# Kernel optimization log

Hardware: AMD Instinct MI355X
Metric: run time of the kernel (lower is better)

## Reference

```python
import jax, jax.numpy as jnp
import numpy as np

B, N, DIN, DOUT, H, DH, DC, NL, L = 8, 256, 64, 64, 8, 8, 64, 32, 2
SCALE = DH ** -0.5  # out_dim-per-head scaling used by both attention variants


def _ln(x, g, b):
    m = jnp.mean(x, -1, keepdims=True)
    v = jnp.mean((x - m) ** 2, -1, keepdims=True)
    return (x - m) * jax.lax.rsqrt(v + 1e-5) * g + b


def _cross_attn(x, ctx, mask_b, wq, wkv, wo, bo):
    # CrossAttentionLayer: standard softmax attention with clamp(-5,5)
    b, n, _ = x.shape
    m = ctx.shape[1]
    q = (x @ wq).reshape(b, n, H, DH).transpose(0, 2, 1, 3)
    k, v = jnp.split(ctx @ wkv, 2, axis=-1)
    k = k.reshape(b, m, H, DH).transpose(0, 2, 1, 3)
    v = v.reshape(b, m, H, DH).transpose(0, 2, 1, 3)
    sim = jnp.einsum('bhid,bhjd->bhij', q, k) * SCALE
    if mask_b is not None:
        sim = jnp.where(mask_b[:, None, None, :], sim, -jnp.finfo(sim.dtype).max)
    sim = jnp.clip(sim, -5.0, 5.0)
    attn = jax.nn.softmax(sim, axis=-1)
    out = jnp.einsum('bhij,bhjd->bhid', attn, v)
    out = out.transpose(0, 2, 1, 3).reshape(b, n, H * DH)
    return out @ wo + bo


def _mha_edge(p, e, k_RW, mask, wq, wk, we, wv):
    # GraphiT MultiHeadAttentionLayer with edge features + k_RW attention PE
    Q = (p @ wq).reshape(B, N, H, DH)
    K = (p @ wk).reshape(B, N, H, DH) * SCALE
    V = (p @ wv).reshape(B, N, H, DH).transpose(0, 2, 1, 3)  # [B,H,N,d]
    E = (e @ we).reshape(B, N, N, H, DH)
    scores = jnp.einsum('bihk,bjhk,bijhk->bhij', Q, K, E)
    scores = jnp.exp(scores - jnp.max(scores, axis=(-2, -1), keepdims=True))
    scores = scores * mask[:, None, :, None] * mask[:, None, None, :]
    scores = scores * k_RW
    denom = jnp.clip(jnp.sum(scores, -1, keepdims=True), 1e-6, None)
    out = jnp.einsum('bhij,bhjd->bhid', scores, V) / denom
    return out.transpose(0, 2, 1, 3).reshape(B, N, H * DH)


def setup_inputs() -> dict:
    key = jax.random.key(0)
    ks = jax.random.split(key, 32)
    rn = lambda k, s: jax.random.normal(k, s, dtype=jnp.float32)
    inp = {
        'h': rn(ks[0], (B, N, DIN)),
        'p': rn(ks[1], (B, N, DIN)),
        'e': rn(ks[2], (B, N, N, DIN)),
        'k_RW': jax.random.uniform(ks[3], (B, 1, N, N), dtype=jnp.float32),
        'queries': rn(ks[4], (B, NL, DC)),
        'mask': jnp.ones((B, N), dtype=jnp.float32),
        # attention_p (MultiHeadAttentionLayer) weights
        'wq_p': rn(ks[5], (DIN, H * DH)) * 0.05,
        'wk_p': rn(ks[6], (DIN, H * DH)) * 0.05,
        'we_p': rn(ks[7], (DIN, H * DH)) * 0.05,
        'wv_p': rn(ks[8], (DIN, H * DH)) * 0.05,
        'wo_p': rn(ks[9], (DOUT, DOUT)) * 0.05,
        # cross_attention_h (queries attend to nodes)
        'cq_wq': rn(ks[10], (DC, H * DH)) * 0.05,
        'cq_wkv': rn(ks[11], (DIN, 2 * H * DH)) * 0.05,
        'cq_wo': rn(ks[12], (H * DH, DC)) * 0.05,
        'cq_bo': jnp.zeros((DC,), dtype=jnp.float32),
        # L_cross latent self-attention layers (stacked)
        'sa_wq': rn(ks[13], (L, DC, H * DH)) * 0.05,
        'sa_wkv': rn(ks[14], (L, DC, 2 * H * DH)) * 0.05,
        'sa_wo': rn(ks[15], (L, H * DH, DC)) * 0.05,
        'sa_bo': jnp.zeros((L, DC), dtype=jnp.float32),
        # O_queries, norms, FFN
        'oq_w': rn(ks[16], (DC, DC)) * 0.05,
        'ln1_g': jnp.ones((DC,), dtype=jnp.float32),
        'ln1_b': jnp.zeros((DC,), dtype=jnp.float32),
        'ffn_w1': rn(ks[17], (DC, 2 * DC)) * 0.05,
        'ffn_w2': rn(ks[18], (2 * DC, DC)) * 0.05,
        'ln2_g': jnp.ones((DC,), dtype=jnp.float32),
        'ln2_b': jnp.zeros((DC,), dtype=jnp.float32),
    }
    return inp


def reference(h, p, e, k_RW, queries, mask,
              wq_p, wk_p, we_p, wv_p, wo_p,
              cq_wq, cq_wkv, cq_wo, cq_bo,
              sa_wq, sa_wkv, sa_wo, sa_bo,
              oq_w, ln1_g, ln1_b, ffn_w1, ffn_w2, ln2_g, ln2_b):
    # forward_p: update positional encoding via edge-modulated attention
    p_attn = _mha_edge(p, e, k_RW, mask, wq_p, wk_p, we_p, wv_p)
    p_new = p + jnp.tanh(p_attn @ wo_p)  # residual, no dropout (eval)
    # combine node features with updated PE (use_node_pe='sum')
    h_c = h + p_new
    mask_b = mask > 0.5
    # perceiver cross-attention: latents attend to nodes
    q = queries + _cross_attn(queries, h_c, mask_b, cq_wq, cq_wkv, cq_wo, cq_bo)
    # L_cross latent self-attention blocks with residual
    for i in range(L):
        q = q + _cross_attn(q, q, None, sa_wq[i], sa_wkv[i], sa_wo[i], sa_bo[i])
    # O_queries projection + layer norm
    q = _ln(q @ oq_w, ln1_g, ln1_b)
    # feed-forward block on queries
    ff = jax.nn.relu(q @ ffn_w1) @ ffn_w2
    q = _ln(q + ff, ln2_g, ln2_b)
    return q
```

## Files before the change

### kernel.cpp

```cpp
#include <hip/hip_runtime.h>
#include <hip/hip_bf16.h>
#include <math.h>

typedef __bf16 bf16x8 __attribute__((ext_vector_type(8)));
typedef float floatx4 __attribute__((ext_vector_type(4)));

#define ATT_SCALE 0.35355339059327373f

__device__ __forceinline__ __bf16 f2b(float x) { return (__bf16)x; }

__global__ void k_proj(const float* __restrict__ p,
                       const float* __restrict__ wq, const float* __restrict__ wk,
                       const float* __restrict__ wv,
                       float* __restrict__ Q, float* __restrict__ Ks,
                       float* __restrict__ V) {
  int blk = blockIdx.x, t = threadIdx.x;
  __shared__ float xr[64];
  xr[t] = p[blk * 64 + t];
  __syncthreads();
  float aq = 0.f, ak = 0.f, av = 0.f;
#pragma unroll 8
  for (int c = 0; c < 64; c++) {
    float x = xr[c];
    aq += x * wq[c * 64 + t];
    ak += x * wk[c * 64 + t];
    av += x * wv[c * 64 + t];
  }
  Q[blk * 64 + t] = aq;
  Ks[blk * 64 + t] = ak * ATT_SCALE;
  V[blk * 64 + t] = av;
}

__global__ __launch_bounds__(256) void k_edge(
    const float* __restrict__ e, const float* __restrict__ we,
    const float* __restrict__ krw, const float* __restrict__ mask,
    const float* __restrict__ hin, const float* __restrict__ pin,
    const float* __restrict__ wo, const float* __restrict__ cq_wkv,
    const float* __restrict__ Q, const float* __restrict__ Ks,
    const float* __restrict__ V, float* __restrict__ Kc, float* __restrict__ Vc) {
  int bi = blockIdx.x;
  int b = bi >> 8;
  int t = threadIdx.x;
  int w = t >> 6, l = t & 63;
  int l15 = l & 15, quad = l >> 4, half8 = (l >> 3) & 1, d = l & 7;

  bf16x8 wfrag[4][2];
#pragma unroll
  for (int nt = 0; nt < 4; nt++)
#pragma unroll
    for (int kc = 0; kc < 2; kc++)
#pragma unroll
      for (int jj = 0; jj < 8; jj++)
        wfrag[nt][kc][jj] = f2b(we[(kc * 32 + quad * 8 + jj) * 64 + nt * 16 + l15]);

  float qv[4];
#pragma unroll
  for (int nt = 0; nt < 4; nt++) qv[nt] = Q[bi * 64 + nt * 16 + l15];
  float mi = mask[bi];

  float aout[4] = {0.f, 0.f, 0.f, 0.f};
  float aden[4] = {0.f, 0.f, 0.f, 0.f};

  for (int mt = 0; mt < 4; mt++) {
    int j0 = w * 64 + mt * 16;
    const float* ep = e + ((long)bi * 256 + j0 + l15) * 64 + quad * 8;
    float4 ea = *reinterpret_cast<const float4*>(ep);
    float4 eb4 = *reinterpret_cast<const float4*>(ep + 4);
    float4 ec = *reinterpret_cast<const float4*>(ep + 32);
    float4 ed4 = *reinterpret_cast<const float4*>(ep + 36);
    bf16x8 a0, a1;
    a0[0] = f2b(ea.x); a0[1] = f2b(ea.y); a0[2] = f2b(ea.z); a0[3] = f2b(ea.w);
    a0[4] = f2b(eb4.x); a0[5] = f2b(eb4.y); a0[6] = f2b(eb4.z); a0[7] = f2b(eb4.w);
    a1[0] = f2b(ec.x); a1[1] = f2b(ec.y); a1[2] = f2b(ec.z); a1[3] = f2b(ec.w);
    a1[4] = f2b(ed4.x); a1[5] = f2b(ed4.y); a1[6] = f2b(ed4.z); a1[7] = f2b(ed4.w);

    int jr0 = j0 + quad * 4;
    float krw_r[4], mj_r[4];
#pragma unroll
    for (int r = 0; r < 4; r++) {
      krw_r[r] = krw[(long)bi * 256 + jr0 + r];
      mj_r[r] = mask[b * 256 + jr0 + r];
    }
#pragma unroll
    for (int nt = 0; nt < 4; nt++) {
      floatx4 acc = {0.f, 0.f, 0.f, 0.f};
      acc = __builtin_amdgcn_mfma_f32_16x16x32_bf16(a0, wfrag[nt][0], acc, 0, 0, 0);
      acc = __builtin_amdgcn_mfma_f32_16x16x32_bf16(a1, wfrag[nt][1], acc, 0, 0, 0);
      int hk = nt * 16 + l15;
      int hbase = hk & 56;
#pragma unroll
      for (int r = 0; r < 4; r++) {
        int jr = jr0 + r;
        float s = acc[r] * qv[nt] * Ks[(b * 256 + jr) * 64 + hk];
        s += __shfl_xor(s, 1);
        s += __shfl_xor(s, 2);
        s += __shfl_xor(s, 4);
        float wg = __expf(s) * krw_r[r] * mj_r[r];
        aden[nt] += wg;
        aout[nt] += wg * V[(b * 256 + jr) * 64 + hbase + d];
      }
    }
  }
#pragma unroll
  for (int nt = 0; nt < 4; nt++) {
    float o = aout[nt], dn = aden[nt];
    o += __shfl_xor(o, 16); o += __shfl_xor(o, 32);
    dn += __shfl_xor(dn, 16); dn += __shfl_xor(dn, 32);
    aout[nt] = o; aden[nt] = dn;
  }

  __shared__ float red[4][64];
  __shared__ float redden[4][8];
  __shared__ float pav[64];
  __shared__ float hcl[64];
  if (l < 16) {
#pragma unroll
    for (int nt = 0; nt < 4; nt++) {
      int head = nt * 2 + half8;
      red[w][head * 8 + d] = aout[nt];
      if (d == 0) redden[w][head] = aden[nt];
    }
  }
  __syncthreads();
  if (t < 64) {
    int head = t >> 3;
    float num = red[0][t] + red[1][t] + red[2][t] + red[3][t];
    float den = redden[0][head] + redden[1][head] + redden[2][head] + redden[3][head];
    num *= mi;
    den = fmaxf(den * mi, 1e-6f);
    pav[t] = num / den;
  }
  __syncthreads();
  if (t < 64) {
    float a = 0.f;
#pragma unroll 8
    for (int c = 0; c < 64; c++) a += pav[c] * wo[c * 64 + t];
    hcl[t] = hin[bi * 64 + t] + pin[bi * 64 + t] + tanhf(a);
  }
  __syncthreads();
  if (t < 128) {
    float a = 0.f;
#pragma unroll 8
    for (int c = 0; c < 64; c++) a += hcl[c] * cq_wkv[c * 128 + t];
    if (t < 64) Kc[bi * 64 + t] = a;
    else        Vc[bi * 64 + t - 64] = a;
  }
}

__global__ __launch_bounds__(1024) void k_tail(
    const float* __restrict__ quer, const float* __restrict__ Kc,
    const float* __restrict__ Vc, const float* __restrict__ mask,
    const float* __restrict__ cq_wq, const float* __restrict__ cq_wo,
    const float* __restrict__ cq_bo,
    const float* __restrict__ sa_wq, const float* __restrict__ sa_wkv,
    const float* __restrict__ sa_wo, const float* __restrict__ sa_bo,
    const float* __restrict__ oq_w, const float* __restrict__ g1,
    const float* __restrict__ b1, const float* __restrict__ w1,
    const float* __restrict__ w2, const float* __restrict__ g2,
    const float* __restrict__ b2v, float* __restrict__ out) {
  int b = blockIdx.x;
  int t = threadIdx.x;

  __shared__ float pool[8704];
  __shared__ float sq[32 * 68];
  __shared__ float sx[32 * 68];
  __shared__ float soc[32 * 68];
  __shared__ float smask[256];

  {
    int r0 = t >> 5, c2 = (t & 31) * 2;
    sq[r0 * 68 + c2]     = quer[b * 2048 + r0 * 64 + c2];
    sq[r0 * 68 + c2 + 1] = quer[b * 2048 + r0 * 64 + c2 + 1];
    if (t < 256) smask[t] = mask[b * 256 + t];
  }
  __syncthreads();

#pragma unroll
  for (int half = 0; half < 2; half++) {
    int o = t + half * 1024, rr = o >> 6, c = o & 63;
    float a = 0.f;
#pragma unroll 8
    for (int k = 0; k < 64; k++) a += sq[rr * 68 + k] * cq_wq[k * 64 + c];
    sx[rr * 68 + c] = a;
  }
  __syncthreads();

  int r = t >> 5, h = (t >> 2) & 7, s = t & 3;
  {
    float qv8[8];
#pragma unroll
    for (int dd = 0; dd < 8; dd++) qv8[dd] = sx[r * 68 + h * 8 + dd];
    float num[8] = {0.f, 0.f, 0.f, 0.f, 0.f, 0.f, 0.f, 0.f};
    float den = 0.f;
    for (int qtr = 0; qtr < 4; qtr++) {
      {
        int jl = t >> 4, c4 = (t & 15) * 4;
        long row = (long)(b * 256 + qtr * 64 + jl) * 64 + c4;
        float4 kk = *reinterpret_cast<const float4*>(Kc + row);
        float4 vv = *reinterpret_cast<const float4*>(Vc + row);
        *reinterpret_cast<float4*>(&pool[jl * 68 + c4]) = kk;
        *reinterpret_cast<float4*>(&pool[64 * 68 + jl * 68 + c4]) = vv;
      }
      __syncthreads();
#pragma unroll
      for (int jj = 0; jj < 16; jj++) {
        int jl = jj * 4 + s;
        const float* kp = &pool[jl * 68 + h * 8];
        float4 k0 = *reinterpret_cast<const float4*>(kp);
        float4 k1 = *reinterpret_cast<const float4*>(kp + 4);
        float sc = qv8[0] * k0.x + qv8[1] * k0.y + qv8[2] * k0.z + qv8[3] * k0.w
                 + qv8[4] * k1.x + qv8[5] * k1.y + qv8[6] * k1.z + qv8[7] * k1.w;
        sc *= ATT_SCALE;
        sc = (smask[qtr * 64 + jl] > 0.5f) ? sc : -1e30f;
        sc = fminf(fmaxf(sc, -5.f), 5.f);
        float ex = __expf(sc);
        den += ex;
        const float* vp = &pool[64 * 68 + jl * 68 + h * 8];
        float4 v0 = *reinterpret_cast<const float4*>(vp);
        float4 v1 = *reinterpret_cast<const float4*>(vp + 4);
        num[0] += ex * v0.x; num[1] += ex * v0.y; num[2] += ex * v0.z; num[3] += ex * v0.w;
        num[4] += ex * v1.x; num[5] += ex * v1.y; num[6] += ex * v1.z; num[7] += ex * v1.w;
      }
      __syncthreads();
    }
    den += __shfl_xor(den, 1); den += __shfl_xor(den, 2);
#pragma unroll
    for (int dd = 0; dd < 8; dd++) {
      float v = num[dd];
      v += __shfl_xor(v, 1); v += __shfl_xor(v, 2);
      num[dd] = v;
    }
    if (s == 0) {
      float inv = 1.f / den;
#pragma unroll
      for (int dd = 0; dd < 8; dd++) soc[r * 68 + h * 8 + dd] = num[dd] * inv;
    }
  }
  __syncthreads();

#pragma unroll
  for (int half = 0; half < 2; half++) {
    int o = t + half * 1024, rr = o >> 6, c = o & 63;
    float a = 0.f;
#pragma unroll 8
    for (int k = 0; k < 64; k++) a += soc[rr * 68 + k] * cq_wo[k * 64 + c];
    sq[rr * 68 + c] += a + cq_bo[c];
  }
  __syncthreads();

  for (int layer = 0; layer < 2; layer++) {
    const float* wql = sa_wq + layer * 4096;
    const float* wkvl = sa_wkv + layer * 8192;
    const float* wol = sa_wo + layer * 4096;
    const float* bol = sa_bo + layer * 64;

#pragma unroll
    for (int half = 0; half < 2; half++) {
      int o = t + half * 1024, rr = o >> 6, c = o & 63;
      float a = 0.f;
#pragma unroll 8
      for (int k = 0; k < 64; k++) a += sq[rr * 68 + k] * wql[k * 64 + c];
      sx[rr * 68 + c] = a;
    }
#pragma unroll
    for (int qu = 0; qu < 4; qu++) {
      int o = t + qu * 1024, rr = o >> 7, c = o & 127;
      float a = 0.f;
#pragma unroll 8
      for (int k = 0; k < 64; k++) a += sq[rr * 68 + k] * wkvl[k * 128 + c];
      if (c < 64) pool[rr * 65 + c] = a;
      else        pool[2080 + rr * 65 + (c - 64)] = a;
    }
    __syncthreads();

    {
      float qv[8];
#pragma unroll
      for (int dd = 0; dd < 8; dd++) qv[dd] = sx[r * 68 + h * 8 + dd];
      float nm[8] = {0.f, 0.f, 0.f, 0.f, 0.f, 0.f, 0.f, 0.f};
      float dn = 0.f;
#pragma unroll
      for (int jj = 0; jj < 8; jj++) {
        int j = jj * 4 + s;
        const float* kp = &pool[j * 65 + h * 8];
        float sc = 0.f;
#pragma unroll
        for (int dd = 0; dd < 8; dd++) sc += qv[dd] * kp[dd];
        sc *= ATT_SCALE;
        sc = fminf(fmaxf(sc, -5.f), 5.f);
        float ex = __expf(sc);
        dn += ex;
        const float* vp = &pool[2080 + j * 65 + h * 8];
#pragma unroll
        for (int dd = 0; dd < 8; dd++) nm[dd] += ex * vp[dd];
      }
      dn += __shfl_xor(dn, 1); dn += __shfl_xor(dn, 2);
#pragma unroll
      for (int dd = 0; dd < 8; dd++) {
        float v = nm[dd];
        v += __shfl_xor(v, 1); v += __shfl_xor(v, 2);
        nm[dd] = v;
      }
      if (s == 0) {
        float inv = 1.f / dn;
#pragma unroll
        for (int dd = 0; dd < 8; dd++) soc[r * 68 + h * 8 + dd] = nm[dd] * inv;
      }
    }
    __syncthreads();

#pragma unroll
    for (int half = 0; half < 2; half++) {
      int o = t + half * 1024, rr = o >> 6, c = o & 63;
      float a = 0.f;
#pragma unroll 8
      for (int k = 0; k < 64; k++) a += soc[rr * 68 + k] * wol[k * 64 + c];
      sq[rr * 68 + c] += a + bol[c];
    }
    __syncthreads();
  }

#pragma unroll
  for (int half = 0; half < 2; half++) {
    int o = t + half * 1024, rr = o >> 6, c = o & 63;
    float a = 0.f;
#pragma unroll 8
    for (int k = 0; k < 64; k++) a += sq[rr * 68 + k] * oq_w[k * 64 + c];
    sx[rr * 68 + c] = a;
  }
  __syncthreads();
  {
    int wv = t >> 6, lc = t & 63;
#pragma unroll
    for (int pass = 0; pass < 2; pass++) {
      int rr = wv + pass * 16;
      float x = sx[rr * 68 + lc];
      float m = x;
      for (int off = 1; off < 64; off <<= 1) m += __shfl_xor(m, off);
      m *= (1.f / 64.f);
      float dv = x - m, vv = dv * dv;
      for (int off = 1; off < 64; off <<= 1) vv += __shfl_xor(vv, off);
      vv *= (1.f / 64.f);
      sx[rr * 68 + lc] = dv * rsqrtf(vv + 1e-5f) * g1[lc] + b1[lc];
    }
  }
  __syncthreads();

#pragma unroll
  for (int qu = 0; qu < 4; qu++) {
    int o = t + qu * 1024, rr = o >> 7, c = o & 127;
    float a = 0.f;
#pragma unroll 8
    for (int k = 0; k < 64; k++) a += sx[rr * 68 + k] * w1[k * 128 + c];
    pool[rr * 128 + c] = fmaxf(a, 0.f);
  }
  __syncthreads();

  {
    int wv = t >> 6, lc = t & 63;
#pragma unroll
    for (int pass = 0; pass < 2; pass++) {
      int rr = wv + pass * 16;
      float ff = 0.f;
#pragma unroll 8
      for (int k = 0; k < 128; k++) ff += pool[rr * 128 + k] * w2[k * 64 + lc];
      float z = sx[rr * 68 + lc] + ff;
      float m2 = z;
      for (int off = 1; off < 64; off <<= 1) m2 += __shfl_xor(m2, off);
      m2 *= (1.f / 64.f);
      float dz = z - m2, v2 = dz * dz;
      for (int off = 1; off < 64; off <<= 1) v2 += __shfl_xor(v2, off);
      v2 *= (1.f / 64.f);
      out[b * 2048 + rr * 64 + lc] = dz * rsqrtf(v2 + 1e-5f) * g2[lc] + b2v[lc];
    }
  }
}

extern "C" void kernel_launch(void* const* d_in, const int* in_sizes, int n_in,
                              void* d_out, int out_size, void* d_ws, size_t ws_size,
                              hipStream_t stream) {
  const float* h_in   = (const float*)d_in[0];
  const float* p_in   = (const float*)d_in[1];
  const float* e_in   = (const float*)d_in[2];
  const float* krw    = (const float*)d_in[3];
  const float* quer   = (const float*)d_in[4];
  const float* mask   = (const float*)d_in[5];
  const float* wq_p   = (const float*)d_in[6];
  const float* wk_p   = (const float*)d_in[7];
  const float* we_p   = (const float*)d_in[8];
  const float* wv_p   = (const float*)d_in[9];
  const float* wo_p   = (const float*)d_in[10];
  const float* cq_wq  = (const float*)d_in[11];
  const float* cq_wkv = (const float*)d_in[12];
  const float* cq_wo  = (const float*)d_in[13];
  const float* cq_bo  = (const float*)d_in[14];
  const float* sa_wq  = (const float*)d_in[15];
  const float* sa_wkv = (const float*)d_in[16];
  const float* sa_wo  = (const float*)d_in[17];
  const float* sa_bo  = (const float*)d_in[18];
  const float* oq_w   = (const float*)d_in[19];
  const float* ln1_g  = (const float*)d_in[20];
  const float* ln1_b  = (const float*)d_in[21];
  const float* ffn_w1 = (const float*)d_in[22];
  const float* ffn_w2 = (const float*)d_in[23];
  const float* ln2_g  = (const float*)d_in[24];
  const float* ln2_b  = (const float*)d_in[25];

  float* ws = (float*)d_ws;
  float* Q  = ws;
  float* Ks = Q + 131072;
  float* V  = Ks + 131072;
  float* Kc = V + 131072;
  float* Vc = Kc + 131072;

  k_proj<<<2048, 64, 0, stream>>>(p_in, wq_p, wk_p, wv_p, Q, Ks, V);
  k_edge<<<2048, 256, 0, stream>>>(e_in, we_p, krw, mask, h_in, p_in, wo_p, cq_wkv,
                                   Q, Ks, V, Kc, Vc);
  k_tail<<<8, 1024, 0, stream>>>(quer, Kc, Vc, mask, cq_wq, cq_wo, cq_bo,
                                 sa_wq, sa_wkv, sa_wo, sa_bo, oq_w,
                                 ln1_g, ln1_b, ffn_w1, ffn_w2, ln2_g, ln2_b,
                                 (float*)d_out);
}
```

Before: 373.9 us.

## Stage tail weights in LDS as bf16 and batch rows per thread in projections

k_proj now computes 8 rows per 256-thread block, so each weight load is reused across 8 rows instead of one. k_tail stages every weight matrix into shared memory as bf16 and has each thread compute 2–4 output rows. Cross-attention K/V tiles are kept in LDS as bf16, and the cq_wo weights are staged while the first K/V tile loads. Unroll pragmas are also removed throughout k_edge. This trades precision in the tail for fewer global weight reads and less LDS traffic, and dropping the unroll pragmas in k_edge may change its code generation.

```diff
diff --git a/kernel.cpp b/kernel.cpp
--- a/kernel.cpp
+++ b/kernel.cpp
@@ -9,26 +9,34 @@
 
 __device__ __forceinline__ __bf16 f2b(float x) { return (__bf16)x; }
 
-__global__ void k_proj(const float* __restrict__ p,
+__global__ __launch_bounds__(256) void k_proj(const float* __restrict__ p,
                        const float* __restrict__ wq, const float* __restrict__ wk,
                        const float* __restrict__ wv,
                        float* __restrict__ Q, float* __restrict__ Ks,
                        float* __restrict__ V) {
   int blk = blockIdx.x, t = threadIdx.x;
-  __shared__ float xr[64];
-  xr[t] = p[blk * 64 + t];
-  __syncthreads();
-  float aq = 0.f, ak = 0.f, av = 0.f;
-#pragma unroll 8
-  for (int c = 0; c < 64; c++) {
-    float x = xr[c];
-    aq += x * wq[c * 64 + t];
-    ak += x * wk[c * 64 + t];
-    av += x * wv[c * 64 + t];
-  }
-  Q[blk * 64 + t] = aq;
-  Ks[blk * 64 + t] = ak * ATT_SCALE;
-  V[blk * 64 + t] = av;
+  __shared__ float xr[8][64];
+  {
+    int rr = t >> 5, cc = (t & 31) * 2;
+    float2 pz = *reinterpret_cast<const float2*>(p + blk * 512 + rr * 64 + cc);
+    xr[rr][cc] = pz.x; xr[rr][cc + 1] = pz.y;
+  }
+  __syncthreads();
+  if (t < 192) {
+    int mat = t >> 6, c = t & 63;
+    const float* w = (mat == 0) ? wq : ((mat == 1) ? wk : wv);
+    float acc[8] = {0.f, 0.f, 0.f, 0.f, 0.f, 0.f, 0.f, 0.f};
+#pragma unroll 8
+    for (int k = 0; k < 64; k++) {
+      float wv_ = w[k * 64 + c];
+#pragma unroll
+      for (int r = 0; r < 8; r++) acc[r] += xr[r][k] * wv_;
+    }
+    float* dst = (mat == 0) ? Q : ((mat == 1) ? Ks : V);
+    float sc = (mat == 1) ? ATT_SCALE : 1.f;
+#pragma unroll
+    for (int r = 0; r < 8; r++) dst[(blk * 8 + r) * 64 + c] = acc[r] * sc;
+  }
 }
 
 __global__ __launch_bounds__(256) void k_edge(
@@ -45,16 +53,12 @@
   int l15 = l & 15, quad = l >> 4, half8 = (l >> 3) & 1, d = l & 7;
 
   bf16x8 wfrag[4][2];
-#pragma unroll
   for (int nt = 0; nt < 4; nt++)
-#pragma unroll
     for (int kc = 0; kc < 2; kc++)
-#pragma unroll
       for (int jj = 0; jj < 8; jj++)
         wfrag[nt][kc][jj] = f2b(we[(kc * 32 + quad * 8 + jj) * 64 + nt * 16 + l15]);
 
   float qv[4];
-#pragma unroll
   for (int nt = 0; nt < 4; nt++) qv[nt] = Q[bi * 64 + nt * 16 + l15];
   float mi = mask[bi];
 
@@ -76,19 +80,16 @@
 
     int jr0 = j0 + quad * 4;
     float krw_r[4], mj_r[4];
-#pragma unroll
     for (int r = 0; r < 4; r++) {
       krw_r[r] = krw[(long)bi * 256 + jr0 + r];
       mj_r[r] = mask[b * 256 + jr0 + r];
     }
-#pragma unroll
     for (int nt = 0; nt < 4; nt++) {
       floatx4 acc = {0.f, 0.f, 0.f, 0.f};
       acc = __builtin_amdgcn_mfma_f32_16x16x32_bf16(a0, wfrag[nt][0], acc, 0, 0, 0);
       acc = __builtin_amdgcn_mfma_f32_16x16x32_bf16(a1, wfrag[nt][1], acc, 0, 0, 0);
       int hk = nt * 16 + l15;
       int hbase = hk & 56;
-#pragma unroll
       for (int r = 0; r < 4; r++) {
         int jr = jr0 + r;
         float s = acc[r] * qv[nt] * Ks[(b * 256 + jr) * 64 + hk];
@@ -101,7 +102,6 @@
       }
     }
   }
-#pragma unroll
   for (int nt = 0; nt < 4; nt++) {
     float o = aout[nt], dn = aden[nt];
     o += __shfl_xor(o, 16); o += __shfl_xor(o, 32);
@@ -114,7 +114,6 @@
   __shared__ float pav[64];
   __shared__ float hcl[64];
   if (l < 16) {
-#pragma unroll
     for (int nt = 0; nt < 4; nt++) {
       int head = nt * 2 + half8;
       red[w][head * 8 + d] = aout[nt];
@@ -133,17 +132,31 @@
   __syncthreads();
   if (t < 64) {
     float a = 0.f;
-#pragma unroll 8
     for (int c = 0; c < 64; c++) a += pav[c] * wo[c * 64 + t];
     hcl[t] = hin[bi * 64 + t] + pin[bi * 64 + t] + tanhf(a);
   }
   __syncthreads();
   if (t < 128) {
     float a = 0.f;
-#pragma unroll 8
     for (int c = 0; c < 64; c++) a += hcl[c] * cq_wkv[c * 128 + t];
     if (t < 64) Kc[bi * 64 + t] = a;
     else        Vc[bi * 64 + t - 64] = a;
+  }
+}
+
+template <int NR, int NC, int ST>
+__device__ __forceinline__ void stage_w(const float* __restrict__ g,
+                                        __bf16* wls, int t) {
+  constexpr int PER = (NR * NC) >> 10;
+  int i0 = t * PER;
+  int k = i0 / NC, c0 = i0 % NC;
+  const float* src = g + k * NC + c0;
+  __bf16* dst = wls + k * ST + c0;
+#pragma unroll
+  for (int m = 0; m < PER; m += 4) {
+    float4 v = *reinterpret_cast<const float4*>(src + m);
+    dst[m] = f2b(v.x); dst[m + 1] = f2b(v.y);
+    dst[m + 2] = f2b(v.z); dst[m + 3] = f2b(v.w);
   }
 }
 
@@ -161,65 +174,76 @@
   int b = blockIdx.x;
   int t = threadIdx.x;
 
-  __shared__ float pool[8704];
   __shared__ float sq[32 * 68];
   __shared__ float sx[32 * 68];
-  __shared__ float soc[32 * 68];
+  __shared__ float pool[6400];
   __shared__ float smask[256];
-
-  {
-    int r0 = t >> 5, c2 = (t & 31) * 2;
-    sq[r0 * 68 + c2]     = quer[b * 2048 + r0 * 64 + c2];
-    sq[r0 * 68 + c2 + 1] = quer[b * 2048 + r0 * 64 + c2 + 1];
+  __shared__ __bf16 wls[8448];
+
+  float* soc = pool + 4160;
+  __bf16* kq = reinterpret_cast<__bf16*>(pool);
+  __bf16* vq = kq + 4096;
+
+  const int rr6 = t >> 6, c6 = t & 63;
+  const int r2 = t >> 5, h = (t >> 2) & 7, s = t & 3;
+
+  {
+    float2 qz = *reinterpret_cast<const float2*>(quer + b * 2048 + (t >> 5) * 64 + (t & 31) * 2);
+    sq[(t >> 5) * 68 + (t & 31) * 2] = qz.x;
+    sq[(t >> 5) * 68 + (t & 31) * 2 + 1] = qz.y;
     if (t < 256) smask[t] = mask[b * 256 + t];
-  }
-  __syncthreads();
-
-#pragma unroll
-  for (int half = 0; half < 2; half++) {
-    int o = t + half * 1024, rr = o >> 6, c = o & 63;
-    float a = 0.f;
-#pragma unroll 8
-    for (int k = 0; k < 64; k++) a += sq[rr * 68 + k] * cq_wq[k * 64 + c];
-    sx[rr * 68 + c] = a;
-  }
-  __syncthreads();
-
-  int r = t >> 5, h = (t >> 2) & 7, s = t & 3;
+    stage_w<64, 64, 66>(cq_wq, wls, t);
+  }
+  __syncthreads();
+
+  {
+    float a0 = 0.f, a1 = 0.f;
+#pragma unroll 8
+    for (int k = 0; k < 64; k++) {
+      float wv = (float)wls[k * 66 + c6];
+      a0 += sq[rr6 * 68 + k] * wv;
+      a1 += sq[(rr6 + 16) * 68 + k] * wv;
+    }
+    sx[rr6 * 68 + c6] = a0;
+    sx[(rr6 + 16) * 68 + c6] = a1;
+  }
+  __syncthreads();
+
+  float num[8] = {0.f, 0.f, 0.f, 0.f, 0.f, 0.f, 0.f, 0.f};
+  float den = 0.f;
   {
     float qv8[8];
 #pragma unroll
-    for (int dd = 0; dd < 8; dd++) qv8[dd] = sx[r * 68 + h * 8 + dd];
-    float num[8] = {0.f, 0.f, 0.f, 0.f, 0.f, 0.f, 0.f, 0.f};
-    float den = 0.f;
+    for (int dd = 0; dd < 8; dd++) qv8[dd] = sx[r2 * 68 + h * 8 + dd];
     for (int qtr = 0; qtr < 4; qtr++) {
       {
-        int jl = t >> 4, c4 = (t & 15) * 4;
-        long row = (long)(b * 256 + qtr * 64 + jl) * 64 + c4;
-        float4 kk = *reinterpret_cast<const float4*>(Kc + row);
-        float4 vv = *reinterpret_cast<const float4*>(Vc + row);
-        *reinterpret_cast<float4*>(&pool[jl * 68 + c4]) = kk;
-        *reinterpret_cast<float4*>(&pool[64 * 68 + jl * 68 + c4]) = vv;
-      }
+        int half = t >> 9, idx = t & 511;
+        int jl = idx >> 3, c0 = (idx & 7) * 8;
+        const float* src = (half ? Vc : Kc) + ((long)(b * 256 + qtr * 64 + jl)) * 64 + c0;
+        __bf16* dst = (half ? vq : kq) + jl * 64 + c0;
+        float4 u = *reinterpret_cast<const float4*>(src);
+        float4 v = *reinterpret_cast<const float4*>(src + 4);
+        dst[0] = f2b(u.x); dst[1] = f2b(u.y); dst[2] = f2b(u.z); dst[3] = f2b(u.w);
+        dst[4] = f2b(v.x); dst[5] = f2b(v.y); dst[6] = f2b(v.z); dst[7] = f2b(v.w);
+      }
+      if (qtr == 0) stage_w<64, 64, 66>(cq_wo, wls, t);
       __syncthreads();
 #pragma unroll
       for (int jj = 0; jj < 16; jj++) {
         int jl = jj * 4 + s;
-        const float* kp = &pool[jl * 68 + h * 8];
-        float4 k0 = *reinterpret_cast<const float4*>(kp);
-        float4 k1 = *reinterpret_cast<const float4*>(kp + 4);
-        float sc = qv8[0] * k0.x + qv8[1] * k0.y + qv8[2] * k0.z + qv8[3] * k0.w
-                 + qv8[4] * k1.x + qv8[5] * k1.y + qv8[6] * k1.z + qv8[7] * k1.w;
+        bf16x8 kk = *reinterpret_cast<const bf16x8*>(kq + jl * 64 + h * 8);
+        float sc = qv8[0] * (float)kk[0] + qv8[1] * (float)kk[1]
+                 + qv8[2] * (float)kk[2] + qv8[3] * (float)kk[3]
+                 + qv8[4] * (float)kk[4] + qv8[5] * (float)kk[5]
+                 + qv8[6] * (float)kk[6] + qv8[7] * (float)kk[7];
         sc *= ATT_SCALE;
         sc = (smask[qtr * 64 + jl] > 0.5f) ? sc : -1e30f;
         sc = fminf(fmaxf(sc, -5.f), 5.f);
         float ex = __expf(sc);
         den += ex;
-        const float* vp = &pool[64 * 68 + jl * 68 + h * 8];
-        float4 v0 = *reinterpret_cast<const float4*>(vp);
-        float4 v1 = *reinterpret_cast<const float4*>(vp + 4);
-        num[0] += ex * v0.x; num[1] += ex * v0.y; num[2] += ex * v0.z; num[3] += ex * v0.w;
-        num[4] += ex * v1.x; num[5] += ex * v1.y; num[6] += ex * v1.z; num[7] += ex * v1.w;
+        bf16x8 vv = *reinterpret_cast<const bf16x8*>(vq + jl * 64 + h * 8);
+#pragma unroll
+        for (int dd = 0; dd < 8; dd++) num[dd] += ex * (float)vv[dd];
       }
       __syncthreads();
     }
@@ -233,18 +257,22 @@
     if (s == 0) {
       float inv = 1.f / den;
 #pragma unroll
-      for (int dd = 0; dd < 8; dd++) soc[r * 68 + h * 8 + dd] = num[dd] * inv;
-    }
-  }
-  __syncthreads();
-
-#pragma unroll
-  for (int half = 0; half < 2; half++) {
-    int o = t + half * 1024, rr = o >> 6, c = o & 63;
-    float a = 0.f;
-#pragma unroll 8
-    for (int k = 0; k < 64; k++) a += soc[rr * 68 + k] * cq_wo[k * 64 + c];
-    sq[rr * 68 + c] += a + cq_bo[c];
+      for (int dd = 0; dd < 8; dd++) soc[r2 * 68 + h * 8 + dd] = num[dd] * inv;
+    }
+  }
+  __syncthreads();
+
+  {
+    float a0 = 0.f, a1 = 0.f;
+#pragma unroll 8
+    for (int k = 0; k < 64; k++) {
+      float wv = (float)wls[k * 66 + c6];
+      a0 += soc[rr6 * 68 + k] * wv;
+      a1 += soc[(rr6 + 16) * 68 + k] * wv;
+    }
+    float bb = cq_bo[c6];
+    sq[rr6 * 68 + c6] += a0 + bb;
+    sq[(rr6 + 16) * 68 + c6] += a1 + bb;
   }
   __syncthreads();
 
@@ -254,43 +282,56 @@
     const float* wol = sa_wo + layer * 4096;
     const float* bol = sa_bo + layer * 64;
 
-#pragma unroll
-    for (int half = 0; half < 2; half++) {
-      int o = t + half * 1024, rr = o >> 6, c = o & 63;
-      float a = 0.f;
-#pragma unroll 8
-      for (int k = 0; k < 64; k++) a += sq[rr * 68 + k] * wql[k * 64 + c];
-      sx[rr * 68 + c] = a;
-    }
-#pragma unroll
-    for (int qu = 0; qu < 4; qu++) {
-      int o = t + qu * 1024, rr = o >> 7, c = o & 127;
-      float a = 0.f;
-#pragma unroll 8
-      for (int k = 0; k < 64; k++) a += sq[rr * 68 + k] * wkvl[k * 128 + c];
-      if (c < 64) pool[rr * 65 + c] = a;
-      else        pool[2080 + rr * 65 + (c - 64)] = a;
-    }
-    __syncthreads();
-
+    stage_w<64, 64, 66>(wql, wls, t);
+    __syncthreads();
     {
-      float qv[8];
-#pragma unroll
-      for (int dd = 0; dd < 8; dd++) qv[dd] = sx[r * 68 + h * 8 + dd];
+      float a0 = 0.f, a1 = 0.f;
+#pragma unroll 8
+      for (int k = 0; k < 64; k++) {
+        float wv = (float)wls[k * 66 + c6];
+        a0 += sq[rr6 * 68 + k] * wv;
+        a1 += sq[(rr6 + 16) * 68 + k] * wv;
+      }
+      sx[rr6 * 68 + c6] = a0;
+      sx[(rr6 + 16) * 68 + c6] = a1;
+    }
+    __syncthreads();
+    stage_w<64, 128, 130>(wkvl, wls, t);
+    __syncthreads();
+    {
+      int rrk = t >> 7, ck = t & 127;
+      float a0 = 0.f, a1 = 0.f, a2 = 0.f, a3 = 0.f;
+#pragma unroll 8
+      for (int k = 0; k < 64; k++) {
+        float wv = (float)wls[k * 130 + ck];
+        a0 += sq[rrk * 68 + k] * wv;
+        a1 += sq[(rrk + 8) * 68 + k] * wv;
+        a2 += sq[(rrk + 16) * 68 + k] * wv;
+        a3 += sq[(rrk + 24) * 68 + k] * wv;
+      }
+      float* dst = (ck < 64) ? (pool + rrk * 65 + ck) : (pool + 2080 + rrk * 65 + (ck - 64));
+      dst[0] = a0; dst[8 * 65] = a1; dst[16 * 65] = a2; dst[24 * 65] = a3;
+    }
+    __syncthreads();
+    {
+      stage_w<64, 64, 66>(wol, wls, t);
+      float qv8[8];
+#pragma unroll
+      for (int dd = 0; dd < 8; dd++) qv8[dd] = sx[r2 * 68 + h * 8 + dd];
       float nm[8] = {0.f, 0.f, 0.f, 0.f, 0.f, 0.f, 0.f, 0.f};
       float dn = 0.f;
 #pragma unroll
       for (int jj = 0; jj < 8; jj++) {
         int j = jj * 4 + s;
-        const float* kp = &pool[j * 65 + h * 8];
+        const float* kp = pool + j * 65 + h * 8;
         float sc = 0.f;
 #pragma unroll
-        for (int dd = 0; dd < 8; dd++) sc += qv[dd] * kp[dd];
+        for (int dd = 0; dd < 8; dd++) sc += qv8[dd] * kp[dd];
         sc *= ATT_SCALE;
         sc = fminf(fmaxf(sc, -5.f), 5.f);
         float ex = __expf(sc);
         dn += ex;
-        const float* vp = &pool[2080 + j * 65 + h * 8];
+        const float* vp = pool + 2080 + j * 65 + h * 8;
 #pragma unroll
         for (int dd = 0; dd < 8; dd++) nm[dd] += ex * vp[dd];
       }
@@ -304,36 +345,44 @@
       if (s == 0) {
         float inv = 1.f / dn;
 #pragma unroll
-        for (int dd = 0; dd < 8; dd++) soc[r * 68 + h * 8 + dd] = nm[dd] * inv;
-      }
-    }
-    __syncthreads();
-
-#pragma unroll
-    for (int half = 0; half < 2; half++) {
-      int o = t + half * 1024, rr = o >> 6, c = o & 63;
-      float a = 0.f;
-#pragma unroll 8
-      for (int k = 0; k < 64; k++) a += soc[rr * 68 + k] * wol[k * 64 + c];
-      sq[rr * 68 + c] += a + bol[c];
-    }
-    __syncthreads();
-  }
-
-#pragma unroll
-  for (int half = 0; half < 2; half++) {
-    int o = t + half * 1024, rr = o >> 6, c = o & 63;
-    float a = 0.f;
-#pragma unroll 8
-    for (int k = 0; k < 64; k++) a += sq[rr * 68 + k] * oq_w[k * 64 + c];
-    sx[rr * 68 + c] = a;
-  }
-  __syncthreads();
-  {
-    int wv = t >> 6, lc = t & 63;
+        for (int dd = 0; dd < 8; dd++) soc[r2 * 68 + h * 8 + dd] = nm[dd] * inv;
+      }
+    }
+    __syncthreads();
+    {
+      float a0 = 0.f, a1 = 0.f;
+#pragma unroll 8
+      for (int k = 0; k < 64; k++) {
+        float wv = (float)wls[k * 66 + c6];
+        a0 += soc[rr6 * 68 + k] * wv;
+        a1 += soc[(rr6 + 16) * 68 + k] * wv;
+      }
+      float bb = bol[c6];
+      sq[rr6 * 68 + c6] += a0 + bb;
+      sq[(rr6 + 16) * 68 + c6] += a1 + bb;
+    }
+    __syncthreads();
+  }
+
+  stage_w<64, 64, 66>(oq_w, wls, t);
+  __syncthreads();
+  {
+    float a0 = 0.f, a1 = 0.f;
+#pragma unroll 8
+    for (int k = 0; k < 64; k++) {
+      float wv = (float)wls[k * 66 + c6];
+      a0 += sq[rr6 * 68 + k] * wv;
+      a1 += sq[(rr6 + 16) * 68 + k] * wv;
+    }
+    sx[rr6 * 68 + c6] = a0;
+    sx[(rr6 + 16) * 68 + c6] = a1;
+  }
+  __syncthreads();
+  {
+    int wv_ = t >> 6, lc = t & 63;
 #pragma unroll
     for (int pass = 0; pass < 2; pass++) {
-      int rr = wv + pass * 16;
+      int rr = wv_ + pass * 16;
       float x = sx[rr * 68 + lc];
       float m = x;
       for (int off = 1; off < 64; off <<= 1) m += __shfl_xor(m, off);
@@ -343,27 +392,36 @@
       vv *= (1.f / 64.f);
       sx[rr * 68 + lc] = dv * rsqrtf(vv + 1e-5f) * g1[lc] + b1[lc];
     }
-  }
-  __syncthreads();
-
-#pragma unroll
-  for (int qu = 0; qu < 4; qu++) {
-    int o = t + qu * 1024, rr = o >> 7, c = o & 127;
-    float a = 0.f;
-#pragma unroll 8
-    for (int k = 0; k < 64; k++) a += sx[rr * 68 + k] * w1[k * 128 + c];
-    pool[rr * 128 + c] = fmaxf(a, 0.f);
-  }
-  __syncthreads();
-
-  {
-    int wv = t >> 6, lc = t & 63;
+    stage_w<64, 128, 130>(w1, wls, t);
+  }
+  __syncthreads();
+  {
+    int rrk = t >> 7, ck = t & 127;
+    float a0 = 0.f, a1 = 0.f, a2 = 0.f, a3 = 0.f;
+#pragma unroll 8
+    for (int k = 0; k < 64; k++) {
+      float wv = (float)wls[k * 130 + ck];
+      a0 += sx[rrk * 68 + k] * wv;
+      a1 += sx[(rrk + 8) * 68 + k] * wv;
+      a2 += sx[(rrk + 16) * 68 + k] * wv;
+      a3 += sx[(rrk + 24) * 68 + k] * wv;
+    }
+    pool[rrk * 128 + ck] = fmaxf(a0, 0.f);
+    pool[(rrk + 8) * 128 + ck] = fmaxf(a1, 0.f);
+    pool[(rrk + 16) * 128 + ck] = fmaxf(a2, 0.f);
+    pool[(rrk + 24) * 128 + ck] = fmaxf(a3, 0.f);
+  }
+  __syncthreads();
+  stage_w<128, 64, 66>(w2, wls, t);
+  __syncthreads();
+  {
+    int wv_ = t >> 6, lc = t & 63;
 #pragma unroll
     for (int pass = 0; pass < 2; pass++) {
-      int rr = wv + pass * 16;
+      int rr = wv_ + pass * 16;
       float ff = 0.f;
 #pragma unroll 8
-      for (int k = 0; k < 128; k++) ff += pool[rr * 128 + k] * w2[k * 64 + lc];
+      for (int k = 0; k < 128; k++) ff += pool[rr * 128 + k] * (float)wls[k * 66 + lc];
       float z = sx[rr * 68 + lc] + ff;
       float m2 = z;
       for (int off = 1; off < 64; off <<= 1) m2 += __shfl_xor(m2, off);
@@ -413,7 +471,7 @@
   float* Kc = V + 131072;
   float* Vc = Kc + 131072;
 
-  k_proj<<<2048, 64, 0, stream>>>(p_in, wq_p, wk_p, wv_p, Q, Ks, V);
+  k_proj<<<256, 256, 0, stream>>>(p_in, wq_p, wk_p, wv_p, Q, Ks, V);
   k_edge<<<2048, 256, 0, stream>>>(e_in, we_p, krw, mask, h_in, p_in, wo_p, cq_wkv,
                                    Q, Ks, V, Kc, Vc);
   k_tail<<<8, 1024, 0, stream>>>(quer, Kc, Vc, mask, cq_wq, cq_wo, cq_bo,
```

Result: faster. 333.2 us (-10.9%).
